# Performance work log

Hardware: AMD Instinct MI355X
Metric: run time of the kernel (lower is better)

Reference implementation:

```python
import jax, jax.numpy as jnp
import numpy as np

B, LAT, H, OUT, S, L = 256, 128, 256, 64, 512, 2


def _lstm_layer(xs, h0, c0, Wih, Whh, bih, bhh):
    # xs: [B, S, in_dim]; PyTorch gate order i, f, g, o
    gx = jnp.einsum('bsi,gi->bsg', xs, Wih) + bih + bhh  # [B,S,4H], precomputed input proj
    gx = jnp.swapaxes(gx, 0, 1)  # [S,B,4H]

    def step(carry, g_t):
        h, c = carry
        g = g_t + h @ Whh.T
        i, f, gg, o = jnp.split(g, 4, axis=-1)
        i, f, o = jax.nn.sigmoid(i), jax.nn.sigmoid(f), jax.nn.sigmoid(o)
        c = f * c + i * jnp.tanh(gg)
        h = o * jnp.tanh(c)
        return (h, c), h

    (_, _), hs = jax.lax.scan(step, (h0, c0), gx)
    return jnp.swapaxes(hs, 0, 1)  # [B,S,H]


def setup_inputs() -> dict:
    key = jax.random.key(0)
    ks = jax.random.split(key, 20)
    sc = 0.05
    d = {
        'z': jax.random.normal(ks[0], (B, LAT), jnp.float32),
        'fc_hidden_w': jax.random.normal(ks[1], (H * L, LAT), jnp.float32) * sc,
        'fc_hidden_b': jnp.zeros((H * L,), jnp.float32),
        'fc_cell_w': jax.random.normal(ks[2], (H * L, LAT), jnp.float32) * sc,
        'fc_cell_b': jnp.zeros((H * L,), jnp.float32),
        'fc_input_w': jax.random.normal(ks[3], (H, LAT), jnp.float32) * sc,
        'fc_input_b': jnp.zeros((H,), jnp.float32),
        'W_ih0': jax.random.normal(ks[4], (4 * H, H), jnp.float32) * sc,
        'W_hh0': jax.random.normal(ks[5], (4 * H, H), jnp.float32) * sc,
        'b_ih0': jnp.zeros((4 * H,), jnp.float32),
        'b_hh0': jnp.zeros((4 * H,), jnp.float32),
        'W_ih1': jax.random.normal(ks[6], (4 * H, H), jnp.float32) * sc,
        'W_hh1': jax.random.normal(ks[7], (4 * H, H), jnp.float32) * sc,
        'b_ih1': jnp.zeros((4 * H,), jnp.float32),
        'b_hh1': jnp.zeros((4 * H,), jnp.float32),
        'fc_output_w': jax.random.normal(ks[8], (OUT, H), jnp.float32) * sc,
        'fc_output_b': jnp.zeros((OUT,), jnp.float32),
    }
    return d


def reference(z, fc_hidden_w, fc_hidden_b, fc_cell_w, fc_cell_b, fc_input_w, fc_input_b,
              W_ih0, W_hh0, b_ih0, b_hh0, W_ih1, W_hh1, b_ih1, b_hh1,
              fc_output_w, fc_output_b):
    # init hidden/cell per layer: view(B, L, H) -> layer axis first
    hidden = (z @ fc_hidden_w.T + fc_hidden_b).reshape(B, L, H)
    cell = (z @ fc_cell_w.T + fc_cell_b).reshape(B, L, H)
    # repeated decoder input (same vector at every timestep)
    x0 = z @ fc_input_w.T + fc_input_b  # [B,H]
    xs = jnp.broadcast_to(x0[:, None, :], (B, S, H))
    h1 = _lstm_layer(xs, hidden[:, 0], cell[:, 0], W_ih0, W_hh0, b_ih0, b_hh0)
    # dropout between layers is inference no-op
    h2 = _lstm_layer(h1, hidden[:, 1], cell[:, 1], W_ih1, W_hh1, b_ih1, b_hh1)
    return h2 @ fc_output_w.T + fc_output_b  # [B,S,OUT]
```

## Files before the change

kernel.cpp:

```cpp
#include <hip/hip_runtime.h>
#include <hip/hip_bf16.h>

#define LAT 128
#define H 256
#define OUTD 64
#define SEQ 512

typedef short bf16x8 __attribute__((ext_vector_type(8)));
typedef float f32x4  __attribute__((ext_vector_type(4)));
typedef unsigned long long u64;
typedef unsigned u32;

__device__ __forceinline__ float sigm(float x)  { return 1.f / (1.f + __expf(-x)); }
__device__ __forceinline__ float tanhf_(float x){ return 1.f - 2.f / (__expf(2.f * x) + 1.f); }

__device__ __forceinline__ short f2bs(float x) {
    __hip_bfloat16 b = __float2bfloat16(x);
    return *reinterpret_cast<short*>(&b);
}
__device__ __forceinline__ float bs2f(unsigned short h) {
    u32 b = ((u32)h) << 16;
    float f; __builtin_memcpy(&f, &b, 4); return f;
}
__device__ __forceinline__ u32 f2pair(float a, float b) {
    return ((u32)(unsigned short)f2bs(b) << 16) | (u32)(unsigned short)f2bs(a);
}
__device__ __forceinline__ bf16x8 pack8(const float* s) {
    bf16x8 v;
    v[0]=f2bs(s[0]); v[1]=f2bs(s[1]); v[2]=f2bs(s[2]); v[3]=f2bs(s[3]);
    v[4]=f2bs(s[4]); v[5]=f2bs(s[5]); v[6]=f2bs(s[6]); v[7]=f2bs(s[7]);
    return v;
}

__device__ __forceinline__ u64 sys_load_u64(const u64* p) {
    return __hip_atomic_load((u64*)p, __ATOMIC_RELAXED, __HIP_MEMORY_SCOPE_SYSTEM);
}
__device__ __forceinline__ void sys_store_u64(u64* p, u64 v) {
    (void)__hip_atomic_exchange(p, v, __ATOMIC_RELAXED, __HIP_MEMORY_SCOPE_SYSTEM);
}

__global__ void lstm_prologue_init(const float* __restrict__ z,
                                   const float* __restrict__ Whid,
                                   const float* __restrict__ bhid,
                                   const float* __restrict__ Wcell,
                                   const float* __restrict__ bcell,
                                   const float* __restrict__ bih1,
                                   const float* __restrict__ bhh1,
                                   u64* __restrict__ h0B1,
                                   u64* __restrict__ h1B1,
                                   float* __restrict__ c0,
                                   float* __restrict__ c1,
                                   float* __restrict__ gxb1)
{
    int t = blockIdx.x * 256 + threadIdx.x;
    if (t < 65536) {
        int layer = t >> 15;
        int tt = t & 32767;
        int b = tt >> 7, cp = tt & 127;
        int colA = layer * H + 2 * cp;
        const float* zr = z + b * LAT;
        const float* wA = Whid + colA * LAT;
        const float* wB = wA + LAT;
        float a0 = bhid[colA], a1 = bhid[colA + 1];
        for (int k = 0; k < LAT; k++) { float zv = zr[k]; a0 += zv * wA[k]; a1 += zv * wB[k]; }
        u64 v = ((u64)(u32)layer << 32) | (u64)f2pair(a0, a1);
        (layer ? h1B1 : h0B1)[b * 128 + cp] = v;
    } else if (t < 196608) {
        int tt = t - 65536;
        int b = tt >> 9, col = tt & 511;
        const float* w  = Wcell + col * LAT;
        const float* zr = z + b * LAT;
        float acc = bcell[col];
        for (int k = 0; k < LAT; k++) acc += zr[k] * w[k];
        if (col < H) c0[b * H + col] = acc;
        else         c1[b * H + (col - H)] = acc;
    } else if (t < 197632) {
        int g = t - 196608;
        gxb1[g] = bih1[g] + bhh1[g];
    }
}

__global__ void lstm_prologue_gx0(const float* __restrict__ z,
                                  const float* __restrict__ Win,
                                  const float* __restrict__ bin,
                                  const float* __restrict__ Wih0,
                                  const float* __restrict__ bih0,
                                  const float* __restrict__ bhh0,
                                  u32* __restrict__ gxb0u)
{
    __shared__ float xs[H];
    const int b = blockIdx.y;
    const int tid = threadIdx.x;
    {
        const float* w  = Win + tid * LAT;
        const float* zr = z + b * LAT;
        float acc = bin[tid];
        for (int k = 0; k < LAT; k++) acc += zr[k] * w[k];
        xs[tid] = acc;
    }
    __syncthreads();
    const int cA = blockIdx.x * 512 + 2 * tid;
    const float* wA = Wih0 + cA * H;
    const float* wB = wA + H;
    float a0 = bih0[cA]     + bhh0[cA];
    float a1 = bih0[cA + 1] + bhh0[cA + 1];
    for (int k = 0; k < H; k++) { float xv = xs[k]; a0 += xv * wA[k]; a1 += xv * wB[k]; }
    gxb0u[b * 512 + blockIdx.x * 256 + tid] = f2pair(a0, a1);
}

__global__ __launch_bounds__(256, 1)
void lstm_persistent(const u32* __restrict__ gxb0u, const float* __restrict__ gxb1,
                     const float* __restrict__ c0g, const float* __restrict__ c1g,
                     u64* __restrict__ h0B0, u64* __restrict__ h0B1,
                     u64* __restrict__ h1B0, u64* __restrict__ h1B1,
                     const float* __restrict__ Whh0, const float* __restrict__ Wih1,
                     const float* __restrict__ Whh1, const float* __restrict__ Wout,
                     const float* __restrict__ bout, float* __restrict__ out)
{
    const int wg = blockIdx.x;
    const int bg = wg >> 4;
    const int j  = wg & 15;
    const int tid  = threadIdx.x;
    const int wave = tid >> 6;
    const int q  = (tid >> 4) & 3;
    const int ln = tid & 15;
    const int mycol = j * 16 + wave * 4 + q;
    const int myb   = bg * 16 + ln;

    __shared__ u32 hs0[2][16 * 132];
    __shared__ u32 hs1[2][16 * 132];

    bf16x8 wf[3][8];
    {
        const float* mats[3] = { Whh0, Wih1, Whh1 };
        const int arow = (ln & 3) * H + j * 16 + wave * 4 + (ln >> 2);
        #pragma unroll
        for (int mm = 0; mm < 3; mm++) {
            const float* s = mats[mm] + arow * H;
            #pragma unroll
            for (int kk = 0; kk < 8; kk++) wf[mm][kk] = pack8(s + kk * 32 + q * 8);
        }
    }
    const bool doOut = (j < 4) && (wave == 0);
    bf16x8 wo[8];
    float bor[4] = {0.f, 0.f, 0.f, 0.f};
    if (doOut) {
        const int orow = j * 16 + ln;
        const float* s = Wout + orow * H;
        #pragma unroll
        for (int kk = 0; kk < 8; kk++) wo[kk] = pack8(s + kk * 32 + q * 8);
        #pragma unroll
        for (int r = 0; r < 4; r++) bor[r] = bout[j * 16 + q * 4 + r];
    }

    float gxr0[4], gxr1[4];
    #pragma unroll
    for (int r = 0; r < 4; r++) {
        u32 v = gxb0u[myb * 512 + ((r * 256 + mycol) >> 1)];
        gxr0[r] = bs2f((unsigned short)((mycol & 1) ? (v >> 16) : (v & 0xFFFFu)));
        gxr1[r] = gxb1[r * 256 + mycol];
    }
    float creg0 = c0g[myb * H + mycol];
    float creg1 = c1g[myb * H + mycol];

    u64* A0 = h0B0 + bg * 2048;
    u64* A1 = h0B1 + bg * 2048;
    u64* B0 = h1B0 + bg * 2048;
    u64* B1 = h1B1 + bg * 2048;

    const int pubslot = ln * 128 + j * 8 + wave * 2 + (q >> 1);
    const bool pubLane = ((q & 1) == 0);

    for (int k = 0; k <= SEQ + 1; k++) {
        const u64* P0 = (k & 1) ? A0 : A1;  u64* C0 = (k & 1) ? A1 : A0;
        const u64* P1 = (k & 1) ? B1 : B0;  u64* C1 = (k & 1) ? B0 : B1;
        const int par = k & 1;

        if (k <= SEQ) {
            u64 v[8];
            bool ok = false; int guard = 0;
            while (!ok && guard < 16384) {
                ok = true;
                #pragma unroll
                for (int i = 0; i < 8; i++) v[i] = sys_load_u64(P0 + i * 256 + tid);
                #pragma unroll
                for (int i = 0; i < 8; i++) ok = ok && ((u32)(v[i] >> 32) == (u32)k);
                guard++;
            }
            u32* dst = hs0[par];
            #pragma unroll
            for (int i = 0; i < 8; i++) { int s = i * 256 + tid; dst[(s >> 7) * 132 + (s & 127)] = (u32)v[i]; }
        }
        __syncthreads();

        bf16x8 hb0[8];
        {
            const unsigned short* b0p = (const unsigned short*)hs0[par];
            #pragma unroll
            for (int kk = 0; kk < 8; kk++)
                hb0[kk] = *(const bf16x8*)(b0p + ln * 264 + kk * 32 + q * 8);
        }

        if (k < SEQ) {
            f32x4 acc = {0.f, 0.f, 0.f, 0.f};
            #pragma unroll
            for (int kk = 0; kk < 8; kk++)
                acc = __builtin_amdgcn_mfma_f32_16x16x32_bf16(wf[0][kk], hb0[kk], acc, 0, 0, 0);
            float i_ = sigm(acc[0] + gxr0[0]);
            float f_ = sigm(acc[1] + gxr0[1]);
            float g_ = tanhf_(acc[2] + gxr0[2]);
            float o_ = sigm(acc[3] + gxr0[3]);
            creg0 = f_ * creg0 + i_ * g_;
            int us = (int)(u32)(unsigned short)f2bs(o_ * tanhf_(creg0));
            int other = __shfl_xor(us, 16);
            if (pubLane) {
                u32 pa = (u32)us | ((u32)other << 16);
                sys_store_u64(C0 + pubslot, ((u64)(u32)(k + 1) << 32) | (u64)pa);
            }
        }

        if (k >= 1) {
            u64 v[8];
            bool ok = false; int guard = 0;
            while (!ok && guard < 16384) {
                ok = true;
                #pragma unroll
                for (int i = 0; i < 8; i++) v[i] = sys_load_u64(P1 + i * 256 + tid);
                #pragma unroll
                for (int i = 0; i < 8; i++) ok = ok && ((u32)(v[i] >> 32) == (u32)k);
                guard++;
            }
            u32* dst = hs1[par];
            #pragma unroll
            for (int i = 0; i < 8; i++) { int s = i * 256 + tid; dst[(s >> 7) * 132 + (s & 127)] = (u32)v[i]; }
        }
        __syncthreads();

        bf16x8 hb1[8];
        {
            const unsigned short* b1p = (const unsigned short*)hs1[par];
            #pragma unroll
            for (int kk = 0; kk < 8; kk++)
                hb1[kk] = *(const bf16x8*)(b1p + ln * 264 + kk * 32 + q * 8);
        }

        if (k >= 1 && k <= SEQ) {
            f32x4 acc = {0.f, 0.f, 0.f, 0.f};
            #pragma unroll
            for (int kk = 0; kk < 8; kk++)
                acc = __builtin_amdgcn_mfma_f32_16x16x32_bf16(wf[1][kk], hb0[kk], acc, 0, 0, 0);
            #pragma unroll
            for (int kk = 0; kk < 8; kk++)
                acc = __builtin_amdgcn_mfma_f32_16x16x32_bf16(wf[2][kk], hb1[kk], acc, 0, 0, 0);
            float i_ = sigm(acc[0] + gxr1[0]);
            float f_ = sigm(acc[1] + gxr1[1]);
            float g_ = tanhf_(acc[2] + gxr1[2]);
            float o_ = sigm(acc[3] + gxr1[3]);
            creg1 = f_ * creg1 + i_ * g_;
            int us = (int)(u32)(unsigned short)f2bs(o_ * tanhf_(creg1));
            int other = __shfl_xor(us, 16);
            if (pubLane) {
                u32 pa = (u32)us | ((u32)other << 16);
                sys_store_u64(C1 + pubslot, ((u64)(u32)(k + 1) << 32) | (u64)pa);
            }
        }

        if (k >= 2 && doOut) {
            f32x4 acc = {0.f, 0.f, 0.f, 0.f};
            #pragma unroll
            for (int kk = 0; kk < 8; kk++)
                acc = __builtin_amdgcn_mfma_f32_16x16x32_bf16(wo[kk], hb1[kk], acc, 0, 0, 0);
            f32x4 res;
            #pragma unroll
            for (int r = 0; r < 4; r++) res[r] = acc[r] + bor[r];
            *(f32x4*)&out[(bg * 16 + ln) * (SEQ * OUTD) + (k - 2) * OUTD + j * 16 + q * 4] = res;
        }
    }
}

extern "C" void kernel_launch(void* const* d_in, const int* in_sizes, int n_in,
                              void* d_out, int out_size, void* d_ws, size_t ws_size,
                              hipStream_t stream) {
    const float* z     = (const float*)d_in[0];
    const float* Whid  = (const float*)d_in[1];
    const float* bhid  = (const float*)d_in[2];
    const float* Wcell = (const float*)d_in[3];
    const float* bcell = (const float*)d_in[4];
    const float* Win   = (const float*)d_in[5];
    const float* bin   = (const float*)d_in[6];
    const float* Wih0  = (const float*)d_in[7];
    const float* Whh0  = (const float*)d_in[8];
    const float* bih0  = (const float*)d_in[9];
    const float* bhh0  = (const float*)d_in[10];
    const float* Wih1  = (const float*)d_in[11];
    const float* Whh1  = (const float*)d_in[12];
    const float* bih1  = (const float*)d_in[13];
    const float* bhh1  = (const float*)d_in[14];
    const float* Wout  = (const float*)d_in[15];
    const float* bout  = (const float*)d_in[16];
    float* out = (float*)d_out;

    u32*   gxb0u = (u32*)d_ws;
    float* gxb1  = (float*)(gxb0u + 131072);
    float* c0    = gxb1 + 1024;
    float* c1    = c0 + 65536;
    u64*   h0B0  = (u64*)(c1 + 65536);
    u64*   h0B1  = h0B0 + 32768;
    u64*   h1B0  = h0B1 + 32768;
    u64*   h1B1  = h1B0 + 32768;

    lstm_prologue_init<<<772, 256, 0, stream>>>(z, Whid, bhid, Wcell, bcell,
                                                bih1, bhh1, h0B1, h1B1, c0, c1, gxb1);
    lstm_prologue_gx0<<<dim3(2, 256), 256, 0, stream>>>(z, Win, bin, Wih0, bih0, bhh0, gxb0u);

    void* kargs[] = { (void*)&gxb0u, (void*)&gxb1, (void*)&c0, (void*)&c1,
                      (void*)&h0B0, (void*)&h0B1, (void*)&h1B0, (void*)&h1B1,
                      (void*)&Whh0, (void*)&Wih1, (void*)&Whh1, (void*)&Wout,
                      (void*)&bout, (void*)&out };
    hipError_t ce = hipLaunchCooperativeKernel((const void*)lstm_persistent,
                                               dim3(256), dim3(256), kargs, 0, stream);
    if (ce != hipSuccess) {
        lstm_persistent<<<256, 256, 0, stream>>>(gxb0u, gxb1, c0, c1,
                                                 h0B0, h0B1, h1B0, h1B1,
                                                 Whh0, Wih1, Whh1, Wout, bout, out);
    }
}
```

Before: 1.571 ms.

## Use agent-scope atomics, prefetch polled hidden states, and remap workgroups across XCDs

Memory scope of the flag/data atomics is narrowed from system to agent, and the exchange becomes a plain atomic store. Polling is restructured: each layer's hidden-state slots are loaded ahead of time (before the MFMA work), only still-pending slots are re-polled, and ready slots go to LDS as soon as they arrive. Workgroup-to-(batch group, column slice) mapping is permuted so members of a batch group are spread differently across dies. The aim is lower inter-workgroup handoff latency per timestep in the persistent recurrence. The cost is more register pressure and more complex spin logic.

```diff
diff --git a/kernel.cpp b/kernel.cpp
--- a/kernel.cpp
+++ b/kernel.cpp
@@ -33,10 +33,10 @@
 }
 
 __device__ __forceinline__ u64 sys_load_u64(const u64* p) {
-    return __hip_atomic_load((u64*)p, __ATOMIC_RELAXED, __HIP_MEMORY_SCOPE_SYSTEM);
+    return __hip_atomic_load((u64*)p, __ATOMIC_RELAXED, __HIP_MEMORY_SCOPE_AGENT);
 }
 __device__ __forceinline__ void sys_store_u64(u64* p, u64 v) {
-    (void)__hip_atomic_exchange(p, v, __ATOMIC_RELAXED, __HIP_MEMORY_SCOPE_SYSTEM);
+    __hip_atomic_store(p, v, __ATOMIC_RELAXED, __HIP_MEMORY_SCOPE_AGENT);
 }
 
 __global__ void lstm_prologue_init(const float* __restrict__ z,
@@ -118,8 +118,8 @@
                      const float* __restrict__ bout, float* __restrict__ out)
 {
     const int wg = blockIdx.x;
-    const int bg = wg >> 4;
-    const int j  = wg & 15;
+    const int bg = (wg & 7) * 2 + (wg >> 7);
+    const int j  = (wg >> 3) & 15;
     const int tid  = threadIdx.x;
     const int wave = tid >> 6;
     const int q  = (tid >> 4) & 3;
@@ -171,25 +171,42 @@
     const int pubslot = ln * 128 + j * 8 + wave * 2 + (q >> 1);
     const bool pubLane = ((q & 1) == 0);
 
+    u64 v0[8], v1[8];
+    unsigned pend0 = 0xFFu;
+    #pragma unroll
+    for (int i = 0; i < 8; i++) v0[i] = sys_load_u64(A1 + i * 256 + tid);
+
     for (int k = 0; k <= SEQ + 1; k++) {
-        const u64* P0 = (k & 1) ? A0 : A1;  u64* C0 = (k & 1) ? A1 : A0;
         const u64* P1 = (k & 1) ? B1 : B0;  u64* C1 = (k & 1) ? B0 : B1;
+        u64* C0 = (k & 1) ? A1 : A0;
         const int par = k & 1;
 
         if (k <= SEQ) {
-            u64 v[8];
-            bool ok = false; int guard = 0;
-            while (!ok && guard < 16384) {
-                ok = true;
+            u32* dst = hs0[par];
+            #pragma unroll
+            for (int i = 0; i < 8; i++) {
+                if (((pend0 >> i) & 1) && ((u32)(v0[i] >> 32) == (u32)k)) {
+                    int s = i * 256 + tid;
+                    dst[(s >> 7) * 132 + (s & 127)] = (u32)v0[i];
+                    pend0 &= ~(1u << i);
+                }
+            }
+            const u64* P0 = (k & 1) ? A0 : A1;
+            int guard = 0;
+            while (pend0 && guard < 16384) {
                 #pragma unroll
-                for (int i = 0; i < 8; i++) v[i] = sys_load_u64(P0 + i * 256 + tid);
+                for (int i = 0; i < 8; i++)
+                    if ((pend0 >> i) & 1) v0[i] = sys_load_u64(P0 + i * 256 + tid);
                 #pragma unroll
-                for (int i = 0; i < 8; i++) ok = ok && ((u32)(v[i] >> 32) == (u32)k);
+                for (int i = 0; i < 8; i++) {
+                    if (((pend0 >> i) & 1) && ((u32)(v0[i] >> 32) == (u32)k)) {
+                        int s = i * 256 + tid;
+                        dst[(s >> 7) * 132 + (s & 127)] = (u32)v0[i];
+                        pend0 &= ~(1u << i);
+                    }
+                }
                 guard++;
             }
-            u32* dst = hs0[par];
-            #pragma unroll
-            for (int i = 0; i < 8; i++) { int s = i * 256 + tid; dst[(s >> 7) * 132 + (s & 127)] = (u32)v[i]; }
         }
         __syncthreads();
 
@@ -199,6 +216,12 @@
             #pragma unroll
             for (int kk = 0; kk < 8; kk++)
                 hb0[kk] = *(const bf16x8*)(b0p + ln * 264 + kk * 32 + q * 8);
+        }
+
+        unsigned pend1 = 0xFFu;
+        if (k >= 1) {
+            #pragma unroll
+            for (int i = 0; i < 8; i++) v1[i] = sys_load_u64(P1 + i * 256 + tid);
         }
 
         if (k < SEQ) {
@@ -220,19 +243,30 @@
         }
 
         if (k >= 1) {
-            u64 v[8];
-            bool ok = false; int guard = 0;
-            while (!ok && guard < 16384) {
-                ok = true;
+            u32* dst = hs1[par];
+            #pragma unroll
+            for (int i = 0; i < 8; i++) {
+                if (((pend1 >> i) & 1) && ((u32)(v1[i] >> 32) == (u32)k)) {
+                    int s = i * 256 + tid;
+                    dst[(s >> 7) * 132 + (s & 127)] = (u32)v1[i];
+                    pend1 &= ~(1u << i);
+                }
+            }
+            int guard = 0;
+            while (pend1 && guard < 16384) {
                 #pragma unroll
-                for (int i = 0; i < 8; i++) v[i] = sys_load_u64(P1 + i * 256 + tid);
+                for (int i = 0; i < 8; i++)
+                    if ((pend1 >> i) & 1) v1[i] = sys_load_u64(P1 + i * 256 + tid);
                 #pragma unroll
-                for (int i = 0; i < 8; i++) ok = ok && ((u32)(v[i] >> 32) == (u32)k);
+                for (int i = 0; i < 8; i++) {
+                    if (((pend1 >> i) & 1) && ((u32)(v1[i] >> 32) == (u32)k)) {
+                        int s = i * 256 + tid;
+                        dst[(s >> 7) * 132 + (s & 127)] = (u32)v1[i];
+                        pend1 &= ~(1u << i);
+                    }
+                }
                 guard++;
             }
-            u32* dst = hs1[par];
-            #pragma unroll
-            for (int i = 0; i < 8; i++) { int s = i * 256 + tid; dst[(s >> 7) * 132 + (s & 127)] = (u32)v[i]; }
         }
         __syncthreads();
 
@@ -242,6 +276,12 @@
             #pragma unroll
             for (int kk = 0; kk < 8; kk++)
                 hb1[kk] = *(const bf16x8*)(b1p + ln * 264 + kk * 32 + q * 8);
+        }
+
+        if (k + 1 <= SEQ) {
+            #pragma unroll
+            for (int i = 0; i < 8; i++) v0[i] = sys_load_u64(C0 + i * 256 + tid);
+            pend0 = 0xFFu;
         }
 
         if (k >= 1 && k <= SEQ) {
```

New measurement: 1.690 ms. +7.6%, slower.
